# Optimization experiments

Measured on AMD Instinct MI355X. Metric: run time of the kernel, lower is better.

The kernel has to match this reference:

```python
import jax, jax.numpy as jnp
import numpy as np
from jax import lax

NPOINTS = 4096
K = 16
BN_EPS = 1e-5


def _fps_idx(pts, npoints):
    """Farthest point sampling indices for one cloud. pts: [N,3] -> [npoints] int32."""
    N = pts.shape[0]

    def body(carry, _):
        dist, last = carry
        d = jnp.sum((pts - pts[last]) ** 2, axis=-1)  # [N]
        dist = jnp.minimum(dist, d)
        nxt = jnp.argmax(dist).astype(jnp.int32)
        return (dist, nxt), nxt

    init = (jnp.full((N,), 1e10, pts.dtype), jnp.array(0, jnp.int32))
    _, rest = lax.scan(body, init, None, length=npoints - 1)
    return jnp.concatenate([jnp.zeros((1,), jnp.int32), rest])


def setup_inputs() -> dict:
    key = jax.random.key(0)
    k1, k2, k3 = jax.random.split(key, 3)
    B, N = 4, 16384
    P, Q = 64, 128
    return {
        "xyz": jax.random.normal(k1, (B, N, 3), jnp.float32),
        "w_planes": jax.random.normal(k2, (P, 3), jnp.float32) * 0.1,   # Conv2d(3->P,1x1,no bias)
        "w_shapes": jax.random.normal(k3, (Q, P), jnp.float32) * 0.1,   # Conv1d(P->Q,1,no bias)
        "bn_gamma": jnp.ones((Q,), jnp.float32),
        "bn_beta": jnp.zeros((Q,), jnp.float32),
        "bn_mean": jnp.zeros((Q,), jnp.float32),
        "bn_var": jnp.ones((Q,), jnp.float32),
    }


def reference(xyz, w_planes, w_shapes, bn_gamma, bn_beta, bn_mean, bn_var):
    # xyz: [B, N, 3]
    # 1) FPS -> xyz_new [B, S, 3]
    fps_idx = jax.vmap(lambda p: _fps_idx(p, NPOINTS))(xyz)            # [B, S]
    xyz_new = jnp.take_along_axis(xyz, fps_idx[:, :, None], axis=1)    # [B, S, 3]

    # 2) KNN of xyz_new in xyz (squared-L2, ascending)
    d = (jnp.sum(xyz_new ** 2, -1)[:, :, None]
         + jnp.sum(xyz ** 2, -1)[:, None, :]
         - 2.0 * jnp.einsum('bsc,bnc->bsn', xyz_new, xyz))             # [B, S, N]
    _, idx = lax.top_k(-d, K)                                          # [B, S, K], nearest first
    idx_nb = idx[:, :, 1:]                                             # drop self -> [B, S, K-1]

    # 3) group_points + center: relative neighbor coords
    knn = jax.vmap(lambda p, i: p[i])(xyz, idx_nb)                     # [B, S, K-1, 3]
    rel = knn - xyz_new[:, :, None, :]                                 # [B, S, K-1, 3]
    nrm = jnp.linalg.norm(rel, axis=-1, keepdims=True) + 1e-8          # [B, S, K-1, 1]

    # 4) 1x1 conv over coords, normalize, weighted max over neighbors
    planes = jnp.einsum('bskc,pc->bskp', rel, w_planes) / nrm          # [B, S, K-1, P]
    planes = jnp.max(nrm * planes * jnp.abs(planes), axis=2)           # [B, S, P]

    # 5) MLP: Conv1d(no bias) + BatchNorm1d(eval) + ReLU
    x = jnp.einsum('bsp,qp->bsq', planes, w_shapes)                    # [B, S, Q]
    x = (x - bn_mean) * (bn_gamma / jnp.sqrt(bn_var + BN_EPS)) + bn_beta
    shapes = jax.nn.relu(x).transpose(0, 2, 1)                         # [B, Q, S]
    return shapes, xyz_new, idx
```

## Files before the change

kernel.cpp:

```cpp
#include <hip/hip_runtime.h>

#define BB 4
#define NN 16384
#define SS 4096
#define KK 16
#define KE 17
#define PP 64
#define QQ 128

#define OFF_XYZNEW 2097152u
#define OFF_IDX    2146304u
#define OUT_ELEMS  2408448u

#define FTH 512
#define FPT (NN / FTH)
#define PAIRS (FPT / 2)
#define NWAVE (FTH / 64)

#define KTH 256
#define NW 4
#define PART (NN / NW)
#define QPB 64
#define NBLK (SS / QPB)
#define CAP 12
#define UU  8
#define MARGIN 1e-3f

typedef float float2v __attribute__((ext_vector_type(2)));

__device__ __forceinline__ float mulrn(float a, float b) { return __fmul_rn(a, b); }
__device__ __forceinline__ float addrn(float a, float b) { return __fadd_rn(a, b); }
__device__ __forceinline__ float subrn(float a, float b) { return __fsub_rn(a, b); }

template<int CTRL>
__device__ __forceinline__ void dpp_amax(float& bv, int& bg)
{
    int vi = __builtin_amdgcn_update_dpp(__float_as_int(bv), __float_as_int(bv),
                                         CTRL, 0xf, 0xf, false);
    int gi = __builtin_amdgcn_update_dpp(bg, bg, CTRL, 0xf, 0xf, false);
    float ov = __int_as_float(vi);
    bool c = (ov > bv) | ((ov == bv) & (gi < bg));
    bg = c ? gi : bg;
    bv = c ? ov : bv;
}

__global__ __launch_bounds__(FTH)
__attribute__((amdgpu_waves_per_eu(2, 2)))
void fps_kernel(
    const float* __restrict__ xyz,
    float* __restrict__ out,
    float* __restrict__ ws, unsigned ws_floats)
{
    const int b   = blockIdx.x;
    const int tid = threadIdx.x;
    const float* base = xyz + (size_t)b * NN * 3;

    float2v pxx[PAIRS], pyy[PAIRS], pzz[PAIRS], pdd[PAIRS];
#pragma unroll
    for (int i = 0; i < PAIRS; ++i) {
        int g0 = tid + FTH * (2 * i);
        int g1 = tid + FTH * (2 * i + 1);
        pxx[i] = (float2v){ base[g0 * 3 + 0], base[g1 * 3 + 0] };
        pyy[i] = (float2v){ base[g0 * 3 + 1], base[g1 * 3 + 1] };
        pzz[i] = (float2v){ base[g0 * 3 + 2], base[g1 * 3 + 2] };
        pdd[i] = (float2v){ 1e10f, 1e10f };
        asm volatile("" : "+v"(pxx[i]));
        asm volatile("" : "+v"(pyy[i]));
        asm volatile("" : "+v"(pzz[i]));
    }

    __shared__ uint2 wvg[2][NWAVE];

    float lx = base[0], ly = base[1], lz = base[2];
    if (tid == 0) {
        unsigned o = OFF_XYZNEW + (unsigned)b * SS * 3u;
        out[o + 0] = lx; out[o + 1] = ly; out[o + 2] = lz;
        unsigned w = (unsigned)b * SS * 3u;
        if (w + 2u < ws_floats) { ws[w] = lx; ws[w + 1] = ly; ws[w + 2] = lz; }
    }

    const int lane = tid & 63;
    const int wave = tid >> 6;
    int p = 0;

    for (int s = 1; s < SS; ++s) {
#pragma clang fp contract(off)
        const float2v lx2 = (float2v){ lx, lx };
        const float2v ly2 = (float2v){ ly, ly };
        const float2v lz2 = (float2v){ lz, lz };
        float bestv = -1.0f;
        int   bj    = 0;
#pragma unroll
        for (int i = 0; i < PAIRS; ++i) {
            float2v dx = pxx[i] - lx2;
            float2v dy = pyy[i] - ly2;
            float2v dz = pzz[i] - lz2;
            float2v dd = (dx * dx + dy * dy) + dz * dz;
            float n0 = fminf(pdd[i].x, dd.x);
            float n1 = fminf(pdd[i].y, dd.y);
            pdd[i] = (float2v){ n0, n1 };
            bj    = (n0 > bestv) ? (2 * i)     : bj;
            bestv = fmaxf(bestv, n0);
            bj    = (n1 > bestv) ? (2 * i + 1) : bj;
            bestv = fmaxf(bestv, n1);
        }
        int bestg = tid + FTH * bj;

        dpp_amax<0x111>(bestv, bestg);
        dpp_amax<0x112>(bestv, bestg);
        dpp_amax<0x114>(bestv, bestg);
        dpp_amax<0x118>(bestv, bestg);
        dpp_amax<0x142>(bestv, bestg);
        dpp_amax<0x143>(bestv, bestg);

        if (lane == 63) wvg[p][wave] = make_uint2(__float_as_uint(bestv), (unsigned)bestg);
        __syncthreads();

        uint2 e0 = wvg[p][0];
        float bv = __uint_as_float(e0.x); int bg = (int)e0.y;
#pragma unroll
        for (int w = 1; w < NWAVE; ++w) {
            uint2 e = wvg[p][w];
            float v = __uint_as_float(e.x); int g = (int)e.y;
            bool c = (v > bv) | ((v == bv) & (g < bg));
            bg = c ? g : bg;
            bv = c ? v : bv;
        }

        int bgu = __builtin_amdgcn_readfirstlane(bg);
        lx = base[bgu * 3 + 0];
        ly = base[bgu * 3 + 1];
        lz = base[bgu * 3 + 2];

        if (tid == 0) {
            unsigned o = OFF_XYZNEW + ((unsigned)b * SS + (unsigned)s) * 3u;
            out[o + 0] = lx; out[o + 1] = ly; out[o + 2] = lz;
            unsigned w = ((unsigned)b * SS + (unsigned)s) * 3u;
            if (w + 2u < ws_floats) { ws[w] = lx; ws[w + 1] = ly; ws[w + 2] = lz; }
        }
        p ^= 1;
    }
}

__global__ __launch_bounds__(KTH) void knn_shape_kernel(
    const float* __restrict__ xyz,
    const float* __restrict__ ws, int use_ws, unsigned ws_floats,
    const float* __restrict__ w_planes, const float* __restrict__ w_shapes,
    const float* __restrict__ bn_gamma, const float* __restrict__ bn_beta,
    const float* __restrict__ bn_mean, const float* __restrict__ bn_var,
    float* __restrict__ out)
{
    __shared__ float sd[CAP][KTH];
    __shared__ int   sg[CAP][KTH];
    __shared__ float wpx[PP], wpy[PP], wpz[PP];
    __shared__ float bsc[QQ], bmn[QQ], bbt[QQ];
    __shared__ int   ski[NW][KE][QPB];
    __shared__ int   ski64[NW][KK][QPB];

    const int tid  = threadIdx.x;
    const int lane = tid & 63;
    const int w    = tid >> 6;
    const int blk  = blockIdx.x;
    const int b    = blk / NBLK;
    const int s    = (blk % NBLK) * QPB + lane;

    for (int i = tid; i < PP; i += KTH) {
        wpx[i] = w_planes[i * 3 + 0];
        wpy[i] = w_planes[i * 3 + 1];
        wpz[i] = w_planes[i * 3 + 2];
    }
    for (int i = tid; i < QQ; i += KTH) {
        bsc[i] = bn_gamma[i] / sqrtf(bn_var[i] + 1e-5f);
        bmn[i] = bn_mean[i];
        bbt[i] = bn_beta[i];
    }
    __syncthreads();

    const float* bx = xyz + (size_t)b * NN * 3;

    float qx, qy, qz;
    {
        unsigned wq = ((unsigned)b * SS + (unsigned)s) * 3u;
        if (use_ws && wq + 2u < ws_floats) {
            qx = ws[wq]; qy = ws[wq + 1]; qz = ws[wq + 2];
        } else {
            unsigned o = OFF_XYZNEW + wq;
            qx = out[o + 0]; qy = out[o + 1]; qz = out[o + 2];
        }
    }
    const float  qsq   = addrn(addrn(mulrn(qx, qx), mulrn(qy, qy)), mulrn(qz, qz));
    const double qxd = (double)qx, qyd = (double)qy, qzd = (double)qz;
    const double qsq64 = qxd * qxd + qyd * qyd + qzd * qzd;

    float  kd[KE];   int ki[KE];
    double kd64[KK]; int ki64[KK];
#pragma unroll
    for (int t = 0; t < KE; ++t) { kd[t] = 3.0e38f; ki[t] = 0; }
#pragma unroll
    for (int t = 0; t < KK; ++t) { kd64[t] = 1.0e300; ki64[t] = 0; }

    int   cnt  = 0;
    float taum = 3.0e38f;

    auto drain = [&]() {
        for (int t = 0; t < CAP; ++t) {
            if (!__any(t < cnt)) break;
            const bool act = t < cnt;
            float d = 0.0f; int g = 0;
            if (act) { d = sd[t][tid]; g = sg[t][tid]; }
            if (act) {
                if (d < kd[KE - 1]) {
                    kd[KE - 1] = d; ki[KE - 1] = g;
#pragma unroll
                    for (int t2 = KE - 1; t2 >= 1; --t2) {
                        if (kd[t2] < kd[t2 - 1]) {
                            float td = kd[t2]; kd[t2] = kd[t2 - 1]; kd[t2 - 1] = td;
                            int   ti = ki[t2]; ki[t2] = ki[t2 - 1]; ki[t2 - 1] = ti;
                        }
                    }
                }
                const float* pg = bx + (size_t)g * 3u;
                float x = pg[0], y = pg[1], z = pg[2];
                double xd = (double)x, yd = (double)y, zd = (double)z;
                double tq64  = xd * xd + yd * yd + zd * zd;
                double dot64 = xd * qxd + yd * qyd + zd * qzd;
                double d64   = qsq64 + tq64 - 2.0 * dot64;
                if (d64 < kd64[KK - 1]) {
                    kd64[KK - 1] = d64; ki64[KK - 1] = g;
#pragma unroll
                    for (int t2 = KK - 1; t2 >= 1; --t2) {
                        if (kd64[t2] < kd64[t2 - 1]) {
                            double td = kd64[t2]; kd64[t2] = kd64[t2 - 1]; kd64[t2 - 1] = td;
                            int    ti = ki64[t2]; ki64[t2] = ki64[t2 - 1]; ki64[t2 - 1] = ti;
                        }
                    }
                }
            }
        }
        cnt  = 0;
        taum = kd[KE - 1] + MARGIN;
    };

    const int gbeg = w * PART;
    for (int g0 = gbeg; g0 < gbeg + PART; g0 += UU) {
        float4 c4[6];
        const float4* p4 = reinterpret_cast<const float4*>(bx + (size_t)g0 * 3u);
#pragma unroll
        for (int i = 0; i < 6; ++i) c4[i] = p4[i];
        const float* cf = reinterpret_cast<const float*>(c4);
#pragma unroll
        for (int u = 0; u < UU; ++u) {
            int g = g0 + u;
            float x = cf[u * 3 + 0];
            float y = cf[u * 3 + 1];
            float z = cf[u * 3 + 2];
            float tq  = addrn(addrn(mulrn(x, x), mulrn(y, y)), mulrn(z, z));
            float dot = fmaf(z, qz, fmaf(y, qy, mulrn(x, qx)));
            float d   = subrn(addrn(qsq, tq), mulrn(2.0f, dot));
            if (d < taum) { sd[cnt][tid] = d; sg[cnt][tid] = g; ++cnt; }
        }
        if (__any(cnt > CAP - UU)) drain();
    }
    drain();

#pragma unroll
    for (int t = 0; t < KE; ++t) ski[w][t][lane] = ki[t];
#pragma unroll
    for (int t = 0; t < KK; ++t) ski64[w][t][lane] = ki64[t];
    __syncthreads();

    if (tid < QPB) {
        float  kdm[KE]; int kim[KE];
        double k64m[KK]; int i64m[KK];
#pragma unroll
        for (int t = 0; t < KE; ++t) { kdm[t] = 3.0e38f; kim[t] = 0; }
#pragma unroll
        for (int t = 0; t < KK; ++t) { k64m[t] = 1.0e300; i64m[t] = 0; }

        for (int w2 = 0; w2 < NW; ++w2) {
            int gs[KE];
#pragma unroll
            for (int t = 0; t < KE; ++t) gs[t] = ski[w2][t][lane];
            for (int a = 1; a < KE; ++a) {
                int key = gs[a]; int bi = a - 1;
                while (bi >= 0 && gs[bi] > key) { gs[bi + 1] = gs[bi]; --bi; }
                gs[bi + 1] = key;
            }
            for (int t = 0; t < KE; ++t) {
                int g = gs[t];
                float x = bx[g * 3 + 0];
                float y = bx[g * 3 + 1];
                float z = bx[g * 3 + 2];
                float tq  = addrn(addrn(mulrn(x, x), mulrn(y, y)), mulrn(z, z));
                float dot = fmaf(z, qz, fmaf(y, qy, mulrn(x, qx)));
                float d   = subrn(addrn(qsq, tq), mulrn(2.0f, dot));
                if (d < kdm[KE - 1]) {
                    kdm[KE - 1] = d; kim[KE - 1] = g;
#pragma unroll
                    for (int t2 = KE - 1; t2 >= 1; --t2) {
                        if (kdm[t2] < kdm[t2 - 1]) {
                            float td = kdm[t2]; kdm[t2] = kdm[t2 - 1]; kdm[t2 - 1] = td;
                            int   ti = kim[t2]; kim[t2] = kim[t2 - 1]; kim[t2 - 1] = ti;
                        }
                    }
                }
            }
        }
        for (int w2 = 0; w2 < NW; ++w2) {
            int gs[KK];
#pragma unroll
            for (int t = 0; t < KK; ++t) gs[t] = ski64[w2][t][lane];
            for (int a = 1; a < KK; ++a) {
                int key = gs[a]; int bi = a - 1;
                while (bi >= 0 && gs[bi] > key) { gs[bi + 1] = gs[bi]; --bi; }
                gs[bi + 1] = key;
            }
            for (int t = 0; t < KK; ++t) {
                int g = gs[t];
                const float* pg = bx + (size_t)g * 3u;
                float x = pg[0], y = pg[1], z = pg[2];
                double xd = (double)x, yd = (double)y, zd = (double)z;
                double tq64  = xd * xd + yd * yd + zd * zd;
                double dot64 = xd * qxd + yd * qyd + zd * qzd;
                double d64   = qsq64 + tq64 - 2.0 * dot64;
                if (d64 < k64m[KK - 1]) {
                    k64m[KK - 1] = d64; i64m[KK - 1] = g;
#pragma unroll
                    for (int t2 = KK - 1; t2 >= 1; --t2) {
                        if (k64m[t2] < k64m[t2 - 1]) {
                            double td = k64m[t2]; k64m[t2] = k64m[t2 - 1]; k64m[t2 - 1] = td;
                            int    ti = i64m[t2]; i64m[t2] = i64m[t2 - 1]; i64m[t2 - 1] = ti;
                        }
                    }
                }
            }
        }

        bool agree = true;
#pragma unroll
        for (int t = 0; t < KK; ++t) agree = agree && (kim[t] == i64m[t]);

        bool hastie = false;
#pragma unroll
        for (int t = 1; t < KE; ++t) hastie = hastie || (kdm[t] == kdm[t - 1]);

        const bool use_f32 = agree || hastie;
        int kf[KK];
#pragma unroll
        for (int t = 0; t < KK; ++t) kf[t] = use_f32 ? kim[t] : i64m[t];

        float pl[PP];
#pragma unroll
        for (int p = 0; p < PP; ++p) pl[p] = -3.0e38f;

        for (int k = 1; k < KK; ++k) {
            int g = kf[k];
            float rx = bx[g * 3 + 0] - qx;
            float ry = bx[g * 3 + 1] - qy;
            float rz = bx[g * 3 + 2] - qz;
            float nrm  = sqrtf(rx * rx + ry * ry + rz * rz) + 1e-8f;
            float invn = 1.0f / nrm;
            for (int p = 0; p < PP; ++p) {
                float t = rx * wpx[p] + ry * wpy[p] + rz * wpz[p];
                float a = t * invn;
                float v = nrm * a * fabsf(a);
                pl[p] = fmaxf(pl[p], v);
            }
        }

        for (int q = 0; q < QQ; ++q) {
            float acc = 0.0f;
            for (int p = 0; p < PP; ++p) acc = fmaf(pl[p], w_shapes[q * PP + p], acc);
            float y2 = (acc - bmn[q]) * bsc[q] + bbt[q];
            y2 = fmaxf(y2, 0.0f);
            unsigned o = ((unsigned)b * QQ + (unsigned)q) * SS + (unsigned)s;
            out[o] = y2;
        }

        for (int t = 0; t < KK; ++t) {
            unsigned o = OFF_IDX + ((unsigned)b * SS + (unsigned)s) * (unsigned)KK + (unsigned)t;
            out[o] = (float)kf[t];
        }
    }
}

extern "C" void kernel_launch(void* const* d_in, const int* in_sizes, int n_in,
                              void* d_out, int out_size, void* d_ws, size_t ws_size,
                              hipStream_t stream)
{
    const float* xyz      = (const float*)d_in[0];
    const float* w_planes = (const float*)d_in[1];
    const float* w_shapes = (const float*)d_in[2];
    const float* bn_gamma = (const float*)d_in[3];
    const float* bn_beta  = (const float*)d_in[4];
    const float* bn_mean  = (const float*)d_in[5];
    const float* bn_var   = (const float*)d_in[6];

    float* out = (float*)d_out;
    float* ws  = (float*)d_ws;

    const unsigned ws_floats = (unsigned)(ws_size / 4);
    const int use_ws = (ws_size >= (size_t)BB * SS * 3 * 4) ? 1 : 0;

    hipLaunchKernelGGL(fps_kernel, dim3(BB), dim3(FTH), 0, stream,
                       xyz, out, ws, ws_floats);

    hipLaunchKernelGGL(knn_shape_kernel, dim3(BB * NBLK), dim3(KTH), 0, stream,
                       xyz, ws, use_ws, ws_floats,
                       w_planes, w_shapes,
                       bn_gamma, bn_beta, bn_mean, bn_var,
                       out);
}
```

Before: 7.396 ms.

## Move FPS x/y coordinates to LDS and drop packed float2 math

The FPS kernel now keeps only z and the running min-distance in registers and stores x and y in shared memory as float4 quads, read back each iteration with 128-bit LDS loads. The packed float2 arithmetic is replaced by scalar round-to-nearest ops with explicit no-contract semantics. The aim is to relieve VGPR pressure and scalarize the math. In exchange, every FPS iteration adds LDS traffic across 4095 serial steps, and packed-math throughput is lost.

Result: slower. 8.293 ms (+12.1%).

```diff
diff --git a/kernel.cpp b/kernel.cpp
--- a/kernel.cpp
+++ b/kernel.cpp
@@ -14,7 +14,7 @@
 
 #define FTH 512
 #define FPT (NN / FTH)
-#define PAIRS (FPT / 2)
+#define NQUAD (FPT / 4)
 #define NWAVE (FTH / 64)
 
 #define KTH 256
@@ -25,8 +25,6 @@
 #define CAP 12
 #define UU  8
 #define MARGIN 1e-3f
-
-typedef float float2v __attribute__((ext_vector_type(2)));
 
 __device__ __forceinline__ float mulrn(float a, float b) { return __fmul_rn(a, b); }
 __device__ __forceinline__ float addrn(float a, float b) { return __fadd_rn(a, b); }
@@ -51,25 +49,32 @@
     float* __restrict__ out,
     float* __restrict__ ws, unsigned ws_floats)
 {
+    __shared__ float4 xs4[NQUAD][FTH];
+    __shared__ float4 ys4[NQUAD][FTH];
+    __shared__ uint2  wvg[2][NWAVE];
+
     const int b   = blockIdx.x;
     const int tid = threadIdx.x;
     const float* base = xyz + (size_t)b * NN * 3;
 
-    float2v pxx[PAIRS], pyy[PAIRS], pzz[PAIRS], pdd[PAIRS];
-#pragma unroll
-    for (int i = 0; i < PAIRS; ++i) {
-        int g0 = tid + FTH * (2 * i);
-        int g1 = tid + FTH * (2 * i + 1);
-        pxx[i] = (float2v){ base[g0 * 3 + 0], base[g1 * 3 + 0] };
-        pyy[i] = (float2v){ base[g0 * 3 + 1], base[g1 * 3 + 1] };
-        pzz[i] = (float2v){ base[g0 * 3 + 2], base[g1 * 3 + 2] };
-        pdd[i] = (float2v){ 1e10f, 1e10f };
-        asm volatile("" : "+v"(pxx[i]));
-        asm volatile("" : "+v"(pyy[i]));
-        asm volatile("" : "+v"(pzz[i]));
-    }
-
-    __shared__ uint2 wvg[2][NWAVE];
+    float pz_[FPT], dist[FPT];
+#pragma unroll
+    for (int k = 0; k < NQUAD; ++k) {
+        float4 xv, yv;
+#pragma unroll
+        for (int u = 0; u < 4; ++u) {
+            int j = 4 * k + u;
+            int g = tid + FTH * j;
+            ((float*)&xv)[u] = base[g * 3 + 0];
+            ((float*)&yv)[u] = base[g * 3 + 1];
+            pz_[j]   = base[g * 3 + 2];
+            dist[j]  = 1e10f;
+        }
+        xs4[k][tid] = xv;
+        ys4[k][tid] = yv;
+    }
+#pragma unroll
+    for (int j = 0; j < FPT; ++j) asm volatile("" : "+v"(pz_[j]));
 
     float lx = base[0], ly = base[1], lz = base[2];
     if (tid == 0) {
@@ -81,28 +86,33 @@
 
     const int lane = tid & 63;
     const int wave = tid >> 6;
+    const unsigned toff = (unsigned)tid * 16u;
     int p = 0;
 
     for (int s = 1; s < SS; ++s) {
-#pragma clang fp contract(off)
-        const float2v lx2 = (float2v){ lx, lx };
-        const float2v ly2 = (float2v){ ly, ly };
-        const float2v lz2 = (float2v){ lz, lz };
+        unsigned o2 = toff;
+        asm volatile("" : "+v"(o2));
+        const char* xbase = (const char*)&xs4[0][0] + o2;
+        const char* ybase = (const char*)&ys4[0][0] + o2;
+
         float bestv = -1.0f;
         int   bj    = 0;
 #pragma unroll
-        for (int i = 0; i < PAIRS; ++i) {
-            float2v dx = pxx[i] - lx2;
-            float2v dy = pyy[i] - ly2;
-            float2v dz = pzz[i] - lz2;
-            float2v dd = (dx * dx + dy * dy) + dz * dz;
-            float n0 = fminf(pdd[i].x, dd.x);
-            float n1 = fminf(pdd[i].y, dd.y);
-            pdd[i] = (float2v){ n0, n1 };
-            bj    = (n0 > bestv) ? (2 * i)     : bj;
-            bestv = fmaxf(bestv, n0);
-            bj    = (n1 > bestv) ? (2 * i + 1) : bj;
-            bestv = fmaxf(bestv, n1);
+        for (int k = 0; k < NQUAD; ++k) {
+            float4 X = *(const float4*)(xbase + (unsigned)k * (FTH * 16u));
+            float4 Y = *(const float4*)(ybase + (unsigned)k * (FTH * 16u));
+#pragma unroll
+            for (int u = 0; u < 4; ++u) {
+                int j = 4 * k + u;
+                float dx = subrn(((const float*)&X)[u], lx);
+                float dy = subrn(((const float*)&Y)[u], ly);
+                float dz = subrn(pz_[j], lz);
+                float d  = addrn(addrn(mulrn(dx, dx), mulrn(dy, dy)), mulrn(dz, dz));
+                float nd = fminf(dist[j], d);
+                dist[j] = nd;
+                bj    = (nd > bestv) ? j : bj;
+                bestv = fmaxf(bestv, nd);
+            }
         }
         int bestg = tid + FTH * bj;
 
```
